# Performance work log

Measured on AMD Instinct MI355X. Metric: run time of the kernel, lower is better.

The kernel has to match this reference:

```python
import jax, jax.numpy as jnp
import numpy as np
import math

IN_DIM = 1024
INTER_DIM = 1024
HIDDEN_DIM = 1024
OUT_DIM = 1024
NUM_GROUPS = 16
N = 8192
EPS = 1e-5


def setup_inputs() -> dict:
    key = jax.random.key(0)
    ks = jax.random.split(key, 20)
    def lin(kw, kb, fan_out, fan_in):
        bound = 1.0 / math.sqrt(fan_in)
        W = jax.random.uniform(kw, (fan_out, fan_in), jnp.float32, -bound, bound)
        b = jax.random.uniform(kb, (fan_out,), jnp.float32, -bound, bound)
        return W, b
    Wq, bq = lin(ks[0], ks[1], INTER_DIM, IN_DIM)
    Wk, bk = lin(ks[2], ks[3], INTER_DIM, IN_DIM)
    Wv, bv = lin(ks[4], ks[5], INTER_DIM, IN_DIM)
    Wr, br = lin(ks[6], ks[7], HIDDEN_DIM, INTER_DIM)
    Wc, bc = lin(ks[8], ks[9], HIDDEN_DIM, OUT_DIM)
    Wp, bp = lin(ks[10], ks[11], OUT_DIM, 2 * HIDDEN_DIM)
    return {
        'h': jax.random.normal(ks[12], (N, IN_DIM), jnp.float32),
        'D': jax.random.uniform(ks[13], (N, N), jnp.float32),
        'h_prime': jax.random.normal(ks[14], (N, OUT_DIM), jnp.float32),
        'Wq': Wq, 'bq': bq, 'Wk': Wk, 'bk': bk, 'Wv': Wv, 'bv': bv,
        'Wr': Wr, 'br': br, 'Wc': Wc, 'bc': bc, 'Wp': Wp, 'bp': bp,
        'prelu_w': jnp.full((OUT_DIM,), 0.25, jnp.float32),
        'gn_w': jnp.ones((OUT_DIM,), jnp.float32),
        'gn_b': jnp.zeros((OUT_DIM,), jnp.float32),
    }


def reference(h, D, h_prime, Wq, bq, Wk, bk, Wv, bv, Wr, br, Wc, bc, Wp, bp, prelu_w, gn_w, gn_b):
    # projections [N, inter]
    Q = h @ Wq.T + bq
    K = h @ Wk.T + bk
    V = h @ Wv.T + bv
    # decay-masked retention: softmax(D * QK^T / sqrt(d)) @ V
    scores = (Q @ K.T) * (1.0 / math.sqrt(INTER_DIM))   # [N, N]
    attn = jax.nn.softmax(D * scores, axis=-1)
    h_ret = attn @ V                                     # [N, inter]
    h_ret = jax.nn.gelu(h_ret @ Wr.T + br, approximate=False)  # [N, hidden]
    h_cat = h_prime @ Wc.T + bc                          # [N, hidden]
    combined = jnp.concatenate([h_ret, h_cat], axis=-1)  # [N, 2*hidden]
    x = combined @ Wp.T + bp                             # [N, out]
    # PReLU (per-channel slope over feature dim)
    x = jnp.where(x >= 0, x, prelu_w[None, :] * x)
    # GroupNorm over (C, N) layout: normalize each group of channels jointly over all N
    xt = x.T                                             # [C, N]
    xg = xt.reshape(NUM_GROUPS, -1)                      # [G, (C/G)*N]
    mean = jnp.mean(xg, axis=1, keepdims=True)
    var = jnp.var(xg, axis=1, keepdims=True)
    xg = (xg - mean) * jax.lax.rsqrt(var + EPS)
    xt = xg.reshape(OUT_DIM, N) * gn_w[:, None] + gn_b[:, None]
    return xt.T                                          # [N, out]
```

## Files before the change

kernel.cpp:

```cpp
#include <hip/hip_runtime.h>
#include <hip/hip_bf16.h>


typedef __bf16 bf16x8 __attribute__((ext_vector_type(8)));
typedef float f32x4 __attribute__((ext_vector_type(4)));
typedef unsigned short ushort_t;
typedef unsigned short ushort8 __attribute__((ext_vector_type(8)));


__device__ __forceinline__ void gload_lds16(const void* g, void* lds) {
  __builtin_amdgcn_global_load_lds((const __attribute__((address_space(1))) void*)g,
                                   (__attribute__((address_space(3))) void*)lds,
                                   16, 0, 0);
}

__device__ __forceinline__ ushort_t f2bu(float x) {
  __hip_bfloat16 h = __float2bfloat16(x);
  return *reinterpret_cast<ushort_t*>(&h);
}

#define FENCE() asm volatile("" ::: "memory")
#define BARRIER() do { FENCE(); __builtin_amdgcn_s_barrier(); FENCE(); } while (0)


__global__ void f2b_kernel(const float* __restrict__ s, __hip_bfloat16* __restrict__ d, int n) {
  const int i4 = (blockIdx.x * 256 + threadIdx.x) * 4;
  if (i4 >= n) return;
  const float4 v = *(const float4*)(s + i4);
  ushort4 o;
  o.x = f2bu(v.x); o.y = f2bu(v.y); o.z = f2bu(v.z); o.w = f2bu(v.w);
  *(ushort4*)((ushort_t*)d + i4) = o;
}

template <int EPI>
__global__ __launch_bounds__(512, 2)
void g8(const __hip_bfloat16* __restrict__ A, const __hip_bfloat16* __restrict__ B,
        __hip_bfloat16* __restrict__ Cb, float* __restrict__ Cf,
        int K, int ldc, int nbnLog2,
        const float* __restrict__ biasN, const float* __restrict__ biasM,
        const float* __restrict__ rowsum, const float* __restrict__ prelu_w,
        float* __restrict__ gstats) {
  __shared__ __align__(16) char ldsm[98304];
  const int tid = threadIdx.x, w = tid >> 6, l = tid & 63;
  const int wm = w >> 2, wn = w & 3;

  const int orig = blockIdx.x;
  const int wg = (orig & 7) * 32 + (orig >> 3);
  const int bm = wg >> nbnLog2, bn = wg & ((1 << nbnLog2) - 1);

  const size_t rowB = (size_t)K * 2;
  const char* Ag = (const char*)A + (size_t)bm * 128 * rowB;
  const char* Bg = (const char*)B + (size_t)bn * 256 * rowB;
  const int NT = K >> 6;

  auto stageU = [&](int p, int unit, const char* srcbase) {
    char* ldsu = ldsm + p * 49152 + unit * 16384;
#pragma unroll
    for (int i = 0; i < 2; ++i) {
      const int cb = i * 512 + w * 64;
      const int c = cb + l;
      const int r = c >> 3;
      const int j = (c & 7) ^ (r & 7);
      gload_lds16(srcbase + (size_t)r * rowB + j * 16, ldsu + cb * 16);
    }
  };
  auto stA = [&](int p, int kt) { stageU(p, 0, Ag + (size_t)kt * 128); };
  auto stB = [&](int p, int hh, int kt) {
    stageU(p, 1 + hh, Bg + (size_t)hh * 128 * rowB + (size_t)kt * 128);
  };

  auto rdA = [&](int p, int f, int kk) -> bf16x8 {
    const int R = wm * 64 + f * 16 + (l & 15);
    const int j = kk * 4 + (l >> 4);
    const int chunk = R * 8 + (j ^ (R & 7));
    return *(const bf16x8*)(ldsm + p * 49152 + chunk * 16);
  };
  auto rdB = [&](int p, int nf, int kk) -> bf16x8 {
    const int Rg = wn * 64 + nf * 16 + (l & 15);
    const int hh = Rg >> 7, Rl = Rg & 127;
    const int j = kk * 4 + (l >> 4);
    const int chunk = Rl * 8 + (j ^ (Rl & 7));
    return *(const bf16x8*)(ldsm + p * 49152 + 16384 + hh * 16384 + chunk * 16);
  };

  stA(0, 0); stB(0, 0, 0); stB(0, 1, 0);
  stA(1, 1);
  asm volatile("s_waitcnt vmcnt(2)" ::: "memory");
  BARRIER();

  f32x4 acc[4][4] = {};
  bf16x8 Af[4][2], Bf[2][2];

#define PH_A_B01(p)                                            \
  _Pragma("unroll") for (int f = 0; f < 4; ++f)                \
  _Pragma("unroll") for (int kk = 0; kk < 2; ++kk)             \
      Af[f][kk] = rdA(p, f, kk);                               \
  _Pragma("unroll") for (int g = 0; g < 2; ++g)                \
  _Pragma("unroll") for (int kk = 0; kk < 2; ++kk)             \
      Bf[g][kk] = rdB(p, g, kk)

#define PH_B23(p)                                              \
  _Pragma("unroll") for (int g = 0; g < 2; ++g)                \
  _Pragma("unroll") for (int kk = 0; kk < 2; ++kk)             \
      Bf[g][kk] = rdB(p, 2 + g, kk)

#define PRE_MFMA()                                             \
  asm volatile("s_waitcnt lgkmcnt(0)" ::: "memory");           \
  __builtin_amdgcn_sched_barrier(0)

#define MF(CB)                                                          \
  __builtin_amdgcn_s_setprio(1);                                        \
  _Pragma("unroll") for (int kk = 0; kk < 2; ++kk)                      \
  _Pragma("unroll") for (int f = 0; f < 4; ++f)                         \
  _Pragma("unroll") for (int g = 0; g < 2; ++g)                         \
      acc[f][(CB) + g] = __builtin_amdgcn_mfma_f32_16x16x32_bf16(       \
          Af[f][kk], Bf[g][kk], acc[f][(CB) + g], 0, 0, 0);             \
  __builtin_amdgcn_s_setprio(0)

#pragma unroll 1
  for (int t = 0; t < NT; t += 2) {
    const bool s2 = (t + 2 < NT);
    PH_A_B01(0);
    stB(1, 0, t + 1); stB(1, 1, t + 1);
    BARRIER(); PRE_MFMA();
    MF(0);
    BARRIER();
    PH_B23(0);
    if (s2) stA(0, t + 2);
    if (s2) asm volatile("s_waitcnt vmcnt(2)" ::: "memory");
    else    asm volatile("s_waitcnt vmcnt(0)" ::: "memory");
    BARRIER(); PRE_MFMA();
    MF(2);
    BARRIER();
    PH_A_B01(1);
    if (s2) { stB(0, 0, t + 2); stB(0, 1, t + 2); }
    BARRIER(); PRE_MFMA();
    MF(0);
    BARRIER();
    PH_B23(1);
    if (s2) {
      stA(1, t + 3);
      asm volatile("s_waitcnt vmcnt(2)" ::: "memory");
    }
    BARRIER(); PRE_MFMA();
    MF(2);
    BARRIER();
  }
#undef PH_A_B01
#undef PH_B23
#undef PRE_MFMA
#undef MF

  const int r0 = bm * 128 + wm * 64, c0 = bn * 256 + wn * 64;
  float gs = 0.f, gq = 0.f;
#pragma unroll
  for (int mf = 0; mf < 4; ++mf) {
#pragma unroll
    for (int i = 0; i < 4; ++i) {
      const int row = r0 + mf * 16 + ((l >> 4) << 2) + i;
      float rscale = 1.0f;
      if (EPI == 3) rscale = 1.0f / rowsum[row];
#pragma unroll
      for (int nf = 0; nf < 4; ++nf) {
        const int col = c0 + nf * 16 + (l & 15);
        float v = acc[mf][nf][i];
        if (EPI == 0) {
          v += biasN[col];
        } else if (EPI == 1) {
          v += biasM[row];
        } else if (EPI == 3) {
          v = v * rscale + biasN[col];
          v = 0.5f * v * (1.0f + erff(v * 0.70710678118654752f));
        } else if (EPI == 4) {
          v += biasN[col];
          v = (v >= 0.f) ? v : prelu_w[col] * v;
        }
        if (EPI == 4) {
          Cf[(size_t)row * ldc + col] = v;
          gs += v; gq += v * v;
        } else {
          Cb[(size_t)row * ldc + col] = __float2bfloat16(v);
        }
      }
    }
  }
  if (EPI == 4) {
#pragma unroll
    for (int m = 1; m < 64; m <<= 1) {
      gs += __shfl_xor(gs, m);
      gq += __shfl_xor(gq, m);
    }
    if (l == 0) {
      const int g = c0 >> 6;
      atomicAdd(&gstats[g * 2 + 0], gs);
      atomicAdd(&gstats[g * 2 + 1], gq);
    }
  }
}

#define EPAD 260
__global__ __launch_bounds__(512, 2)
void pkern8(const __hip_bfloat16* __restrict__ Q, const __hip_bfloat16* __restrict__ Kmat,
            const float* __restrict__ D, __hip_bfloat16* __restrict__ P,
            float* __restrict__ rowsum, int nt) {
  __shared__ __align__(16) char ldsm[133120];
  const int tid = threadIdx.x, w = tid >> 6, l = tid & 63;
  const int wm = w >> 2, wn = w & 3;

  const int orig = blockIdx.x;
  const int wg = (orig & 7) * 128 + (orig >> 3);
  const int bm = wg >> 5, bn = wg & 31;

  const char* Ag = (const char*)Q + (size_t)bm * 256 * 2048;
  const char* Bg = (const char*)Kmat + (size_t)bn * 256 * 2048;

  auto stage = [&](int p, int ab, int hh, int kt) {
    const char* srcbase = (ab ? Bg : Ag) + (size_t)hh * 128 * 2048 + (size_t)kt * 128;
    char* ldsbase = ldsm + p * 65536 + ab * 32768 + hh * 16384;
#pragma unroll
    for (int i = 0; i < 2; ++i) {
      const int cbase = i * 512 + w * 64;
      const int c = cbase + l;
      const int r = c >> 3;
      const int j = (c & 7) ^ (r & 7);
      gload_lds16(srcbase + (size_t)r * 2048 + j * 16, ldsbase + cbase * 16);
    }
  };

  auto rdA = [&](int p, int mh, int kk, int f) -> bf16x8 {
    const int R = mh * 64 + f * 16 + (l & 15);
    const int j = kk * 4 + (l >> 4);
    const int chunk = R * 8 + (j ^ (R & 7));
    return *(const bf16x8*)(ldsm + p * 65536 + wm * 16384 + chunk * 16);
  };
  auto rdB = [&](int p, int nh, int kk, int g) -> bf16x8 {
    const int R = (wn & 1) * 64 + (nh * 2 + g) * 16 + (l & 15);
    const int j = kk * 4 + (l >> 4);
    const int chunk = R * 8 + (j ^ (R & 7));
    return *(const bf16x8*)(ldsm + p * 65536 + 32768 + (wn >> 1) * 16384 + chunk * 16);
  };

  stage(0, 0, 0, 0); stage(0, 0, 1, 0); stage(0, 1, 0, 0); stage(0, 1, 1, 0);
  stage(1, 1, 0, 1); stage(1, 0, 0, 1); stage(1, 0, 1, 1);
  asm volatile("s_waitcnt vmcnt(6)" ::: "memory");
  BARRIER();

  f32x4 acc[8][4] = {};
  bf16x8 Af[4][2], B0[2][2], B1[2][2];

#define MFMA_QUAD(RB, CB, BREG)                                                          \
  __builtin_amdgcn_s_setprio(1);                                                         \
  _Pragma("unroll") for (int kk = 0; kk < 2; ++kk)                                       \
  _Pragma("unroll") for (int f = 0; f < 4; ++f)                                          \
  _Pragma("unroll") for (int g = 0; g < 2; ++g)                                          \
      acc[(RB) + f][(CB) + g] = __builtin_amdgcn_mfma_f32_16x16x32_bf16(                 \
          Af[f][kk], BREG[g][kk], acc[(RB) + f][(CB) + g], 0, 0, 0);                     \
  __builtin_amdgcn_s_setprio(0)

#define PRE_MFMA()                                           \
  asm volatile("s_waitcnt lgkmcnt(0)" ::: "memory");         \
  __builtin_amdgcn_sched_barrier(0)

#define RD_A(p, mh)                                          \
  _Pragma("unroll") for (int f = 0; f < 4; ++f)              \
  _Pragma("unroll") for (int kk = 0; kk < 2; ++kk)           \
      Af[f][kk] = rdA(p, mh, kk, f)

#define RD_B(p, nh, DST)                                     \
  _Pragma("unroll") for (int g = 0; g < 2; ++g)              \
  _Pragma("unroll") for (int kk = 0; kk < 2; ++kk)           \
      DST[g][kk] = rdB(p, nh, kk, g)

#pragma unroll 1
  for (int t = 0; t < nt; t += 2) {
    const bool s2 = (t + 2 < nt), s3 = (t + 3 < nt);
    RD_A(0, 0); RD_B(0, 0, B0);
    stage(1, 1, 1, t + 1);
    BARRIER(); PRE_MFMA();
    MFMA_QUAD(0, 0, B0);
    BARRIER();

    RD_B(0, 1, B1);
    BARRIER(); PRE_MFMA();
    MFMA_QUAD(0, 2, B1);
    BARRIER();

    RD_A(0, 1);
    if (s2) stage(0, 1, 0, t + 2);
    BARRIER(); PRE_MFMA();
    MFMA_QUAD(4, 2, B1);
    BARRIER();

    if (s2) stage(0, 0, 0, t + 2);
    if (s2) asm volatile("s_waitcnt vmcnt(4)" ::: "memory");
    else    asm volatile("s_waitcnt vmcnt(0)" ::: "memory");
    BARRIER(); PRE_MFMA();
    MFMA_QUAD(4, 0, B0);
    BARRIER();

    RD_A(1, 0); RD_B(1, 0, B0);
    if (s2) stage(0, 0, 1, t + 2);
    BARRIER(); PRE_MFMA();
    MFMA_QUAD(0, 0, B0);
    BARRIER();

    RD_B(1, 1, B1);
    if (s2) stage(0, 1, 1, t + 2);
    BARRIER(); PRE_MFMA();
    MFMA_QUAD(0, 2, B1);
    BARRIER();

    RD_A(1, 1);
    if (s3) stage(1, 1, 0, t + 3);
    BARRIER(); PRE_MFMA();
    MFMA_QUAD(4, 2, B1);
    BARRIER();

    if (s3) { stage(1, 0, 0, t + 3); stage(1, 0, 1, t + 3); }
    asm volatile("s_waitcnt vmcnt(6)" ::: "memory");
    BARRIER(); PRE_MFMA();
    MFMA_QUAD(4, 0, B0);
    BARRIER();
  }
#undef MFMA_QUAD
#undef PRE_MFMA
#undef RD_A
#undef RD_B

  float* lds32 = (float*)ldsm;
  const int rbase = bm * 256, cb = bn * 256;
  const int rl = tid >> 5;
  const int cl = (tid & 31) * 8;
#pragma unroll 1
  for (int h = 0; h < 2; ++h) {
    float4 dreg[16];
#pragma unroll
    for (int it = 0; it < 8; ++it) {
      const size_t gof = (size_t)(rbase + h * 128 + it * 16 + rl) * 8192 + (cb + cl);
      dreg[2 * it]     = *(const float4*)(D + gof);
      dreg[2 * it + 1] = *(const float4*)(D + gof + 4);
    }
    BARRIER();
    if (wm == h) {
#pragma unroll
      for (int mf = 0; mf < 8; ++mf)
#pragma unroll
        for (int nf = 0; nf < 4; ++nf)
#pragma unroll
          for (int i = 0; i < 4; ++i)
            lds32[(mf * 16 + ((l >> 4) << 2) + i) * EPAD + (wn * 64 + nf * 16 + (l & 15))] =
                acc[mf][nf][i];
    }
    asm volatile("s_waitcnt lgkmcnt(0)" ::: "memory");
    BARRIER();
#pragma unroll
    for (int it = 0; it < 8; ++it) {
      const int rr = it * 16 + rl;
      const int row = rbase + h * 128 + rr;
      const size_t gof = (size_t)row * 8192 + (cb + cl);
      const float4 s0 = *(const float4*)(lds32 + rr * EPAD + cl);
      const float4 s1 = *(const float4*)(lds32 + rr * EPAD + cl + 4);
      const float4 d0 = dreg[2 * it], d1 = dreg[2 * it + 1];
      float p0 = __expf(d0.x * (s0.x * 0.03125f));
      float p1 = __expf(d0.y * (s0.y * 0.03125f));
      float p2 = __expf(d0.z * (s0.z * 0.03125f));
      float p3 = __expf(d0.w * (s0.w * 0.03125f));
      float p4 = __expf(d1.x * (s1.x * 0.03125f));
      float p5 = __expf(d1.y * (s1.y * 0.03125f));
      float p6 = __expf(d1.z * (s1.z * 0.03125f));
      float p7 = __expf(d1.w * (s1.w * 0.03125f));
      ushort8 o;
      o[0] = f2bu(p0); o[1] = f2bu(p1); o[2] = f2bu(p2); o[3] = f2bu(p3);
      o[4] = f2bu(p4); o[5] = f2bu(p5); o[6] = f2bu(p6); o[7] = f2bu(p7);
      *(ushort8*)((ushort_t*)P + gof) = o;
      float rs = ((p0 + p1) + (p2 + p3)) + ((p4 + p5) + (p6 + p7));
      rs += __shfl_xor(rs, 1); rs += __shfl_xor(rs, 2);
      rs += __shfl_xor(rs, 4); rs += __shfl_xor(rs, 8);
      rs += __shfl_xor(rs, 16);
      if ((tid & 31) == 0) atomicAdd(&rowsum[row], rs);
    }
  }
}
#undef EPAD


__global__ void gn_finalize(const float* __restrict__ x, const float* __restrict__ gstats,
                            const float* __restrict__ gw, const float* __restrict__ gb,
                            float* __restrict__ out, int n) {
  __shared__ float sm[16], sr[16];
  if (threadIdx.x < 16) {
    const float cnt = 64.0f * 8192.0f;
    const float s = gstats[threadIdx.x * 2 + 0];
    const float q = gstats[threadIdx.x * 2 + 1];
    const float mean = s / cnt;
    const float var = q / cnt - mean * mean;
    sm[threadIdx.x] = mean;
    sr[threadIdx.x] = rsqrtf(var + 1e-5f);
  }
  __syncthreads();
  const int i4 = (blockIdx.x * 256 + threadIdx.x) * 4;
  if (i4 >= n) return;
  const float4 v = *(const float4*)(x + i4);
  const int c = i4 & 1023;
  const int g = c >> 6;
  const float mean = sm[g], r = sr[g];
  float4 o;
  o.x = (v.x - mean) * r * gw[c + 0] + gb[c + 0];
  o.y = (v.y - mean) * r * gw[c + 1] + gb[c + 1];
  o.z = (v.z - mean) * r * gw[c + 2] + gb[c + 2];
  o.w = (v.w - mean) * r * gw[c + 3] + gb[c + 3];
  *(float4*)(out + i4) = o;
}


extern "C" void kernel_launch(void* const* d_in, const int* in_sizes, int n_in,
                              void* d_out, int out_size, void* d_ws, size_t ws_size,
                              hipStream_t stream) {
  const float* h  = (const float*)d_in[0];
  const float* D  = (const float*)d_in[1];
  const float* hp = (const float*)d_in[2];
  const float* Wq = (const float*)d_in[3];
  const float* bq = (const float*)d_in[4];
  const float* Wk = (const float*)d_in[5];
  const float* bk = (const float*)d_in[6];
  const float* Wv = (const float*)d_in[7];
  const float* bv = (const float*)d_in[8];
  const float* Wr = (const float*)d_in[9];
  const float* br = (const float*)d_in[10];
  const float* Wc = (const float*)d_in[11];
  const float* bc = (const float*)d_in[12];
  const float* Wp = (const float*)d_in[13];
  const float* bp = (const float*)d_in[14];
  const float* pw = (const float*)d_in[15];
  const float* gw = (const float*)d_in[16];
  const float* gb = (const float*)d_in[17];
  float* out = (float*)d_out;

  char* ws = (char*)d_ws;
  size_t off = 0;
  auto alloc = [&](size_t b) {
    char* p = ws + off;
    off += (b + 255) & ~(size_t)255;
    return p;
  };
  __hip_bfloat16* hb   = (__hip_bfloat16*)alloc(8192ull * 1024 * 2);
  __hip_bfloat16* hpb  = (__hip_bfloat16*)alloc(8192ull * 1024 * 2);
  __hip_bfloat16* Wqb  = (__hip_bfloat16*)alloc(1024ull * 1024 * 2);
  __hip_bfloat16* Wkb  = (__hip_bfloat16*)alloc(1024ull * 1024 * 2);
  __hip_bfloat16* Wvb  = (__hip_bfloat16*)alloc(1024ull * 1024 * 2);
  __hip_bfloat16* Wrb  = (__hip_bfloat16*)alloc(1024ull * 1024 * 2);
  __hip_bfloat16* Wcb  = (__hip_bfloat16*)alloc(1024ull * 1024 * 2);
  __hip_bfloat16* Wpb  = (__hip_bfloat16*)alloc(1024ull * 2048 * 2);
  __hip_bfloat16* Qb   = (__hip_bfloat16*)alloc(8192ull * 1024 * 2);
  __hip_bfloat16* Kb   = (__hip_bfloat16*)alloc(8192ull * 1024 * 2);
  __hip_bfloat16* Vt   = (__hip_bfloat16*)alloc(1024ull * 8192 * 2);
  __hip_bfloat16* R0   = (__hip_bfloat16*)alloc(8192ull * 1024 * 2);
  __hip_bfloat16* comb = (__hip_bfloat16*)alloc(8192ull * 2048 * 2);
  __hip_bfloat16* P    = (__hip_bfloat16*)alloc(8192ull * 8192 * 2);
  float* xbuf   = (float*)alloc(8192ull * 1024 * 4);
  float* rowsum = (float*)alloc(8192ull * 4);
  float* gstats = (float*)alloc(128);
  if (off > ws_size) return;

  hipMemsetAsync(rowsum, 0, 8192 * 4, stream);
  hipMemsetAsync(gstats, 0, 128, stream);

  auto cvt = [&](const float* s, __hip_bfloat16* d, int n) {
    f2b_kernel<<<dim3((n / 4 + 255) / 256), dim3(256), 0, stream>>>(s, d, n);
  };
  cvt(h, hb, 8192 * 1024);
  cvt(hp, hpb, 8192 * 1024);
  cvt(Wq, Wqb, 1024 * 1024);
  cvt(Wk, Wkb, 1024 * 1024);
  cvt(Wv, Wvb, 1024 * 1024);
  cvt(Wr, Wrb, 1024 * 1024);
  cvt(Wc, Wcb, 1024 * 1024);
  cvt(Wp, Wpb, 1024 * 2048);

  g8<0><<<dim3(256), 512, 0, stream>>>(hb, Wqb, Qb, nullptr, 1024, 1024, 2, bq, nullptr, nullptr, nullptr, nullptr);
  g8<0><<<dim3(256), 512, 0, stream>>>(hb, Wkb, Kb, nullptr, 1024, 1024, 2, bk, nullptr, nullptr, nullptr, nullptr);
  g8<1><<<dim3(256), 512, 0, stream>>>(Wvb, hb, Vt, nullptr, 1024, 8192, 5, nullptr, bv, nullptr, nullptr, nullptr);
  pkern8<<<dim3(1024), 512, 0, stream>>>(Qb, Kb, D, P, rowsum, 16);
  g8<2><<<dim3(256), 512, 0, stream>>>(P, Vt, R0, nullptr, 8192, 1024, 2, nullptr, nullptr, nullptr, nullptr, nullptr);
  g8<3><<<dim3(256), 512, 0, stream>>>(R0, Wrb, comb, nullptr, 1024, 2048, 2, br, nullptr, rowsum, nullptr, nullptr);
  g8<0><<<dim3(256), 512, 0, stream>>>(hpb, Wcb, comb + 1024, nullptr, 1024, 2048, 2, bc, nullptr, nullptr, nullptr, nullptr);
  g8<4><<<dim3(256), 512, 0, stream>>>(comb, Wpb, nullptr, xbuf, 2048, 1024, 2, bp, nullptr, nullptr, pw, gstats);
  gn_finalize<<<dim3(8192), 256, 0, stream>>>(xbuf, gstats, gw, gb, out, 8192 * 1024);
}
```

Baseline: 618.5 us.

## Triple-buffer GEMM k-loop and prefetch D tile before QK^T main loop

The bf16 GEMM kernel's split-phase double-buffered k-loop is replaced by a three-buffer ring. Each iteration reads a whole 64-wide k-tile, issues the global-to-LDS loads two tiles ahead, and needs only one barrier. This raises LDS use to 144 KB per block. In the score/exp kernel, the first half of the D tile is loaded into registers before the QK^T loop so its latency overlaps the matrix math. The second half is loaded between the two epilogue passes. The D prefetch keeps 64 extra VGPRs live across the MFMA loop, which risks spilling or lower occupancy.

```diff
diff --git a/kernel.cpp b/kernel.cpp
--- a/kernel.cpp
+++ b/kernel.cpp
@@ -34,13 +34,13 @@
 
 template <int EPI>
 __global__ __launch_bounds__(512, 2)
-void g8(const __hip_bfloat16* __restrict__ A, const __hip_bfloat16* __restrict__ B,
-        __hip_bfloat16* __restrict__ Cb, float* __restrict__ Cf,
-        int K, int ldc, int nbnLog2,
-        const float* __restrict__ biasN, const float* __restrict__ biasM,
-        const float* __restrict__ rowsum, const float* __restrict__ prelu_w,
-        float* __restrict__ gstats) {
-  __shared__ __align__(16) char ldsm[98304];
+void g1p(const __hip_bfloat16* __restrict__ A, const __hip_bfloat16* __restrict__ B,
+         __hip_bfloat16* __restrict__ Cb, float* __restrict__ Cf,
+         int K, int ldc, int nbnLog2,
+         const float* __restrict__ biasN, const float* __restrict__ biasM,
+         const float* __restrict__ rowsum, const float* __restrict__ prelu_w,
+         float* __restrict__ gstats) {
+  __shared__ __align__(16) char ldsm[147456];
   const int tid = threadIdx.x, w = tid >> 6, l = tid & 63;
   const int wm = w >> 2, wn = w & 3;
 
@@ -53,8 +53,7 @@
   const char* Bg = (const char*)B + (size_t)bn * 256 * rowB;
   const int NT = K >> 6;
 
-  auto stageU = [&](int p, int unit, const char* srcbase) {
-    char* ldsu = ldsm + p * 49152 + unit * 16384;
+  auto stageU = [&](char* ldsu, const char* srcbase) {
 #pragma unroll
     for (int i = 0; i < 2; ++i) {
       const int cb = i * 512 + w * 64;
@@ -64,92 +63,65 @@
       gload_lds16(srcbase + (size_t)r * rowB + j * 16, ldsu + cb * 16);
     }
   };
-  auto stA = [&](int p, int kt) { stageU(p, 0, Ag + (size_t)kt * 128); };
-  auto stB = [&](int p, int hh, int kt) {
-    stageU(p, 1 + hh, Bg + (size_t)hh * 128 * rowB + (size_t)kt * 128);
-  };
-
-  auto rdA = [&](int p, int f, int kk) -> bf16x8 {
+  auto stT = [&](char* buf, int kt) {
+    stageU(buf, Ag + (size_t)kt * 128);
+    stageU(buf + 16384, Bg + (size_t)kt * 128);
+    stageU(buf + 32768, Bg + (size_t)128 * rowB + (size_t)kt * 128);
+  };
+
+  auto rdA = [&](const char* buf, int f, int kk) -> bf16x8 {
     const int R = wm * 64 + f * 16 + (l & 15);
     const int j = kk * 4 + (l >> 4);
     const int chunk = R * 8 + (j ^ (R & 7));
-    return *(const bf16x8*)(ldsm + p * 49152 + chunk * 16);
-  };
-  auto rdB = [&](int p, int nf, int kk) -> bf16x8 {
+    return *(const bf16x8*)(buf + chunk * 16);
+  };
+  auto rdB = [&](const char* buf, int nf, int kk) -> bf16x8 {
     const int Rg = wn * 64 + nf * 16 + (l & 15);
     const int hh = Rg >> 7, Rl = Rg & 127;
     const int j = kk * 4 + (l >> 4);
     const int chunk = Rl * 8 + (j ^ (Rl & 7));
-    return *(const bf16x8*)(ldsm + p * 49152 + 16384 + hh * 16384 + chunk * 16);
-  };
-
-  stA(0, 0); stB(0, 0, 0); stB(0, 1, 0);
-  stA(1, 1);
-  asm volatile("s_waitcnt vmcnt(2)" ::: "memory");
+    return *(const bf16x8*)(buf + 16384 + hh * 16384 + chunk * 16);
+  };
+
+  char* pa = ldsm;
+  char* pb = ldsm + 49152;
+  char* pc = ldsm + 98304;
+
+  stT(pa, 0); stT(pb, 1);
+  asm volatile("s_waitcnt vmcnt(6)" ::: "memory");
   BARRIER();
 
   f32x4 acc[4][4] = {};
-  bf16x8 Af[4][2], Bf[2][2];
-
-#define PH_A_B01(p)                                            \
-  _Pragma("unroll") for (int f = 0; f < 4; ++f)                \
-  _Pragma("unroll") for (int kk = 0; kk < 2; ++kk)             \
-      Af[f][kk] = rdA(p, f, kk);                               \
-  _Pragma("unroll") for (int g = 0; g < 2; ++g)                \
-  _Pragma("unroll") for (int kk = 0; kk < 2; ++kk)             \
-      Bf[g][kk] = rdB(p, g, kk)
-
-#define PH_B23(p)                                              \
-  _Pragma("unroll") for (int g = 0; g < 2; ++g)                \
-  _Pragma("unroll") for (int kk = 0; kk < 2; ++kk)             \
-      Bf[g][kk] = rdB(p, 2 + g, kk)
-
-#define PRE_MFMA()                                             \
-  asm volatile("s_waitcnt lgkmcnt(0)" ::: "memory");           \
-  __builtin_amdgcn_sched_barrier(0)
-
-#define MF(CB)                                                          \
-  __builtin_amdgcn_s_setprio(1);                                        \
-  _Pragma("unroll") for (int kk = 0; kk < 2; ++kk)                      \
-  _Pragma("unroll") for (int f = 0; f < 4; ++f)                         \
-  _Pragma("unroll") for (int g = 0; g < 2; ++g)                         \
-      acc[f][(CB) + g] = __builtin_amdgcn_mfma_f32_16x16x32_bf16(       \
-          Af[f][kk], Bf[g][kk], acc[f][(CB) + g], 0, 0, 0);             \
-  __builtin_amdgcn_s_setprio(0)
+  bf16x8 Af[4][2], Bf[4][2];
 
 #pragma unroll 1
-  for (int t = 0; t < NT; t += 2) {
-    const bool s2 = (t + 2 < NT);
-    PH_A_B01(0);
-    stB(1, 0, t + 1); stB(1, 1, t + 1);
-    BARRIER(); PRE_MFMA();
-    MF(0);
-    BARRIER();
-    PH_B23(0);
-    if (s2) stA(0, t + 2);
-    if (s2) asm volatile("s_waitcnt vmcnt(2)" ::: "memory");
-    else    asm volatile("s_waitcnt vmcnt(0)" ::: "memory");
-    BARRIER(); PRE_MFMA();
-    MF(2);
-    BARRIER();
-    PH_A_B01(1);
-    if (s2) { stB(0, 0, t + 2); stB(0, 1, t + 2); }
-    BARRIER(); PRE_MFMA();
-    MF(0);
-    BARRIER();
-    PH_B23(1);
-    if (s2) {
-      stA(1, t + 3);
-      asm volatile("s_waitcnt vmcnt(2)" ::: "memory");
-    }
-    BARRIER(); PRE_MFMA();
-    MF(2);
-    BARRIER();
-  }
-#undef PH_A_B01
-#undef PH_B23
-#undef PRE_MFMA
-#undef MF
+  for (int t = 0; t < NT; ++t) {
+    const bool s1 = (t + 1 < NT), s2 = (t + 2 < NT);
+#pragma unroll
+    for (int f = 0; f < 4; ++f)
+#pragma unroll
+      for (int kk = 0; kk < 2; ++kk) Af[f][kk] = rdA(pa, f, kk);
+#pragma unroll
+    for (int nf = 0; nf < 4; ++nf)
+#pragma unroll
+      for (int kk = 0; kk < 2; ++kk) Bf[nf][kk] = rdB(pa, nf, kk);
+    if (s2) stT(pc, t + 2);
+    asm volatile("s_waitcnt lgkmcnt(0)" ::: "memory");
+    __builtin_amdgcn_sched_barrier(0);
+    __builtin_amdgcn_s_setprio(1);
+#pragma unroll
+    for (int kk = 0; kk < 2; ++kk)
+#pragma unroll
+      for (int f = 0; f < 4; ++f)
+#pragma unroll
+        for (int g = 0; g < 4; ++g)
+          acc[f][g] = __builtin_amdgcn_mfma_f32_16x16x32_bf16(Af[f][kk], Bf[g][kk], acc[f][g], 0, 0, 0);
+    __builtin_amdgcn_s_setprio(0);
+    if (s2)      asm volatile("s_waitcnt vmcnt(6)" ::: "memory");
+    else if (s1) asm volatile("s_waitcnt vmcnt(0)" ::: "memory");
+    BARRIER();
+    char* tmp = pa; pa = pb; pb = pc; pc = tmp;
+  }
 
   const int r0 = bm * 128 + wm * 64, c0 = bn * 256 + wn * 64;
   float gs = 0.f, gq = 0.f;
@@ -214,6 +186,17 @@
   const char* Ag = (const char*)Q + (size_t)bm * 256 * 2048;
   const char* Bg = (const char*)Kmat + (size_t)bn * 256 * 2048;
 
+  const int rl = tid >> 5, cl = (tid & 31) * 8;
+  const int rbase = bm * 256, cb0 = bn * 256;
+  float4 dreg[16];
+#pragma unroll
+  for (int it = 0; it < 8; ++it) {
+    const size_t gof = (size_t)(rbase + it * 16 + rl) * 8192 + (cb0 + cl);
+    dreg[2 * it]     = *(const float4*)(D + gof);
+    dreg[2 * it + 1] = *(const float4*)(D + gof + 4);
+  }
+  __builtin_amdgcn_sched_barrier(0);
+
   auto stage = [&](int p, int ab, int hh, int kt) {
     const char* srcbase = (ab ? Bg : Ag) + (size_t)hh * 128 * 2048 + (size_t)kt * 128;
     char* ldsbase = ldsm + p * 65536 + ab * 32768 + hh * 16384;
@@ -328,57 +311,90 @@
 #undef RD_B
 
   float* lds32 = (float*)ldsm;
-  const int rbase = bm * 256, cb = bn * 256;
-  const int rl = tid >> 5;
-  const int cl = (tid & 31) * 8;
-#pragma unroll 1
-  for (int h = 0; h < 2; ++h) {
-    float4 dreg[16];
-#pragma unroll
-    for (int it = 0; it < 8; ++it) {
-      const size_t gof = (size_t)(rbase + h * 128 + it * 16 + rl) * 8192 + (cb + cl);
-      dreg[2 * it]     = *(const float4*)(D + gof);
-      dreg[2 * it + 1] = *(const float4*)(D + gof + 4);
-    }
-    BARRIER();
-    if (wm == h) {
-#pragma unroll
-      for (int mf = 0; mf < 8; ++mf)
-#pragma unroll
-        for (int nf = 0; nf < 4; ++nf)
-#pragma unroll
-          for (int i = 0; i < 4; ++i)
-            lds32[(mf * 16 + ((l >> 4) << 2) + i) * EPAD + (wn * 64 + nf * 16 + (l & 15))] =
-                acc[mf][nf][i];
-    }
-    asm volatile("s_waitcnt lgkmcnt(0)" ::: "memory");
-    BARRIER();
-#pragma unroll
-    for (int it = 0; it < 8; ++it) {
-      const int rr = it * 16 + rl;
-      const int row = rbase + h * 128 + rr;
-      const size_t gof = (size_t)row * 8192 + (cb + cl);
-      const float4 s0 = *(const float4*)(lds32 + rr * EPAD + cl);
-      const float4 s1 = *(const float4*)(lds32 + rr * EPAD + cl + 4);
-      const float4 d0 = dreg[2 * it], d1 = dreg[2 * it + 1];
-      float p0 = __expf(d0.x * (s0.x * 0.03125f));
-      float p1 = __expf(d0.y * (s0.y * 0.03125f));
-      float p2 = __expf(d0.z * (s0.z * 0.03125f));
-      float p3 = __expf(d0.w * (s0.w * 0.03125f));
-      float p4 = __expf(d1.x * (s1.x * 0.03125f));
-      float p5 = __expf(d1.y * (s1.y * 0.03125f));
-      float p6 = __expf(d1.z * (s1.z * 0.03125f));
-      float p7 = __expf(d1.w * (s1.w * 0.03125f));
-      ushort8 o;
-      o[0] = f2bu(p0); o[1] = f2bu(p1); o[2] = f2bu(p2); o[3] = f2bu(p3);
-      o[4] = f2bu(p4); o[5] = f2bu(p5); o[6] = f2bu(p6); o[7] = f2bu(p7);
-      *(ushort8*)((ushort_t*)P + gof) = o;
-      float rs = ((p0 + p1) + (p2 + p3)) + ((p4 + p5) + (p6 + p7));
-      rs += __shfl_xor(rs, 1); rs += __shfl_xor(rs, 2);
-      rs += __shfl_xor(rs, 4); rs += __shfl_xor(rs, 8);
-      rs += __shfl_xor(rs, 16);
-      if ((tid & 31) == 0) atomicAdd(&rowsum[row], rs);
-    }
+  BARRIER();
+  if (wm == 0) {
+#pragma unroll
+    for (int mf = 0; mf < 8; ++mf)
+#pragma unroll
+      for (int nf = 0; nf < 4; ++nf)
+#pragma unroll
+        for (int i = 0; i < 4; ++i)
+          lds32[(mf * 16 + ((l >> 4) << 2) + i) * EPAD + (wn * 64 + nf * 16 + (l & 15))] =
+              acc[mf][nf][i];
+  }
+  asm volatile("s_waitcnt lgkmcnt(0)" ::: "memory");
+  BARRIER();
+#pragma unroll
+  for (int it = 0; it < 8; ++it) {
+    const int rr = it * 16 + rl;
+    const int row = rbase + rr;
+    const size_t gof = (size_t)row * 8192 + (cb0 + cl);
+    const float4 s0 = *(const float4*)(lds32 + rr * EPAD + cl);
+    const float4 s1 = *(const float4*)(lds32 + rr * EPAD + cl + 4);
+    const float4 d0 = dreg[2 * it], d1 = dreg[2 * it + 1];
+    float p0 = __expf(d0.x * (s0.x * 0.03125f));
+    float p1 = __expf(d0.y * (s0.y * 0.03125f));
+    float p2 = __expf(d0.z * (s0.z * 0.03125f));
+    float p3 = __expf(d0.w * (s0.w * 0.03125f));
+    float p4 = __expf(d1.x * (s1.x * 0.03125f));
+    float p5 = __expf(d1.y * (s1.y * 0.03125f));
+    float p6 = __expf(d1.z * (s1.z * 0.03125f));
+    float p7 = __expf(d1.w * (s1.w * 0.03125f));
+    ushort8 o;
+    o[0] = f2bu(p0); o[1] = f2bu(p1); o[2] = f2bu(p2); o[3] = f2bu(p3);
+    o[4] = f2bu(p4); o[5] = f2bu(p5); o[6] = f2bu(p6); o[7] = f2bu(p7);
+    *(ushort8*)((ushort_t*)P + gof) = o;
+    float rs = ((p0 + p1) + (p2 + p3)) + ((p4 + p5) + (p6 + p7));
+    rs += __shfl_xor(rs, 1); rs += __shfl_xor(rs, 2);
+    rs += __shfl_xor(rs, 4); rs += __shfl_xor(rs, 8);
+    rs += __shfl_xor(rs, 16);
+    if ((tid & 31) == 0) atomicAdd(&rowsum[row], rs);
+  }
+  float4 dreg2[16];
+#pragma unroll
+  for (int it = 0; it < 8; ++it) {
+    const size_t gof = (size_t)(rbase + 128 + it * 16 + rl) * 8192 + (cb0 + cl);
+    dreg2[2 * it]     = *(const float4*)(D + gof);
+    dreg2[2 * it + 1] = *(const float4*)(D + gof + 4);
+  }
+  BARRIER();
+  if (wm == 1) {
+#pragma unroll
+    for (int mf = 0; mf < 8; ++mf)
+#pragma unroll
+      for (int nf = 0; nf < 4; ++nf)
+#pragma unroll
+        for (int i = 0; i < 4; ++i)
+          lds32[(mf * 16 + ((l >> 4) << 2) + i) * EPAD + (wn * 64 + nf * 16 + (l & 15))] =
+              acc[mf][nf][i];
+  }
+  asm volatile("s_waitcnt lgkmcnt(0)" ::: "memory");
+  BARRIER();
+#pragma unroll
+  for (int it = 0; it < 8; ++it) {
+    const int rr = it * 16 + rl;
+    const int row = rbase + 128 + rr;
+    const size_t gof = (size_t)row * 8192 + (cb0 + cl);
+    const float4 s0 = *(const float4*)(lds32 + rr * EPAD + cl);
+    const float4 s1 = *(const float4*)(lds32 + rr * EPAD + cl + 4);
+    const float4 d0 = dreg2[2 * it], d1 = dreg2[2 * it + 1];
+    float p0 = __expf(d0.x * (s0.x * 0.03125f));
+    float p1 = __expf(d0.y * (s0.y * 0.03125f));
+    float p2 = __expf(d0.z * (s0.z * 0.03125f));
+    float p3 = __expf(d0.w * (s0.w * 0.03125f));
+    float p4 = __expf(d1.x * (s1.x * 0.03125f));
+    float p5 = __expf(d1.y * (s1.y * 0.03125f));
+    float p6 = __expf(d1.z * (s1.z * 0.03125f));
+    float p7 = __expf(d1.w * (s1.w * 0.03125f));
+    ushort8 o;
+    o[0] = f2bu(p0); o[1] = f2bu(p1); o[2] = f2bu(p2); o[3] = f2bu(p3);
+    o[4] = f2bu(p4); o[5] = f2bu(p5); o[6] = f2bu(p6); o[7] = f2bu(p7);
+    *(ushort8*)((ushort_t*)P + gof) = o;
+    float rs = ((p0 + p1) + (p2 + p3)) + ((p4 + p5) + (p6 + p7));
+    rs += __shfl_xor(rs, 1); rs += __shfl_xor(rs, 2);
+    rs += __shfl_xor(rs, 4); rs += __shfl_xor(rs, 8);
+    rs += __shfl_xor(rs, 16);
+    if ((tid & 31) == 0) atomicAdd(&rowsum[row], rs);
   }
 }
 #undef EPAD
@@ -477,13 +493,13 @@
   cvt(Wc, Wcb, 1024 * 1024);
   cvt(Wp, Wpb, 1024 * 2048);
 
-  g8<0><<<dim3(256), 512, 0, stream>>>(hb, Wqb, Qb, nullptr, 1024, 1024, 2, bq, nullptr, nullptr, nullptr, nullptr);
-  g8<0><<<dim3(256), 512, 0, stream>>>(hb, Wkb, Kb, nullptr, 1024, 1024, 2, bk, nullptr, nullptr, nullptr, nullptr);
-  g8<1><<<dim3(256), 512, 0, stream>>>(Wvb, hb, Vt, nullptr, 1024, 8192, 5, nullptr, bv, nullptr, nullptr, nullptr);
+  g1p<0><<<dim3(256), 512, 0, stream>>>(hb, Wqb, Qb, nullptr, 1024, 1024, 2, bq, nullptr, nullptr, nullptr, nullptr);
+  g1p<0><<<dim3(256), 512, 0, stream>>>(hb, Wkb, Kb, nullptr, 1024, 1024, 2, bk, nullptr, nullptr, nullptr, nullptr);
+  g1p<1><<<dim3(256), 512, 0, stream>>>(Wvb, hb, Vt, nullptr, 1024, 8192, 5, nullptr, bv, nullptr, nullptr, nullptr);
   pkern8<<<dim3(1024), 512, 0, stream>>>(Qb, Kb, D, P, rowsum, 16);
-  g8<2><<<dim3(256), 512, 0, stream>>>(P, Vt, R0, nullptr, 8192, 1024, 2, nullptr, nullptr, nullptr, nullptr, nullptr);
-  g8<3><<<dim3(256), 512, 0, stream>>>(R0, Wrb, comb, nullptr, 1024, 2048, 2, br, nullptr, rowsum, nullptr, nullptr);
-  g8<0><<<dim3(256), 512, 0, stream>>>(hpb, Wcb, comb + 1024, nullptr, 1024, 2048, 2, bc, nullptr, nullptr, nullptr, nullptr);
-  g8<4><<<dim3(256), 512, 0, stream>>>(comb, Wpb, nullptr, xbuf, 2048, 1024, 2, bp, nullptr, nullptr, pw, gstats);
+  g1p<2><<<dim3(256), 512, 0, stream>>>(P, Vt, R0, nullptr, 8192, 1024, 2, nullptr, nullptr, nullptr, nullptr, nullptr);
+  g1p<3><<<dim3(256), 512, 0, stream>>>(R0, Wrb, comb, nullptr, 1024, 2048, 2, br, nullptr, rowsum, nullptr, nullptr);
+  g1p<0><<<dim3(256), 512, 0, stream>>>(hpb, Wcb, comb + 1024, nullptr, 1024, 2048, 2, bc, nullptr, nullptr, nullptr, nullptr);
+  g1p<4><<<dim3(256), 512, 0, stream>>>(comb, Wpb, nullptr, xbuf, 2048, 1024, 2, bp, nullptr, nullptr, pw, gstats);
   gn_finalize<<<dim3(8192), 256, 0, stream>>>(xbuf, gstats, gw, gb, out, 8192 * 1024);
 }
```

Result: faster. 596.3 us (-3.6%).
